# Optimization experiments

Hardware: AMD Instinct MI355X
Metric: run time of the kernel (lower is better)

The kernel has to match this reference:

```python
import jax, jax.numpy as jnp
import numpy as np
import math

ATTN_TEMP = 2.0


def _make_proj(p):
    # p: (B,2,4,4) -> combined (B,4,4): ext with top 3x4 replaced by K@ext[:3,:4]
    ext, intr = p[:, 0], p[:, 1]
    top = jnp.matmul(intr[:, :3, :3], ext[:, :3, :4])  # (B,3,4)
    return ext.at[:, :3, :4].set(top)


def _warp_grid(src_proj, ref_proj, depth):
    # returns pixel coords (ix, iy) each (B, D*H*W); matches torch homo_warping grid (no grad)
    B, D, H, W = depth.shape
    proj = jnp.matmul(src_proj, jnp.linalg.inv(ref_proj))  # (B,4,4)
    rot, trans = proj[:, :3, :3], proj[:, :3, 3:4]
    y, x = jnp.meshgrid(jnp.arange(H, dtype=jnp.float32), jnp.arange(W, dtype=jnp.float32), indexing='ij')
    xyz = jnp.stack([x.reshape(-1), y.reshape(-1), jnp.ones(H * W, jnp.float32)])  # (3,HW)
    rot_xyz = jnp.einsum('bij,jn->bin', rot, xyz)  # (B,3,HW)
    pxyz = rot_xyz[:, :, None, :] * depth.reshape(B, 1, D, H * W) + trans[:, :, :, None]  # (B,3,D,HW)
    z = pxyz[:, 2]
    z = jnp.where(z == 0, 1e-9, z)
    return jax.lax.stop_gradient((pxyz[:, 0] / z).reshape(B, -1)), jax.lax.stop_gradient((pxyz[:, 1] / z).reshape(B, -1))


def _bilinear_zeros(fea, ix_n, iy_n):
    # fea (B,C,Hs,Ws); ix_n,iy_n normalized [-1,1], align_corners=True, zero padding -> (B,C,N)
    B, C, Hs, Ws = fea.shape
    ix = (ix_n + 1.0) * ((Ws - 1) / 2.0)
    iy = (iy_n + 1.0) * ((Hs - 1) / 2.0)
    x0 = jnp.floor(ix); y0 = jnp.floor(iy)
    wx1 = ix - x0; wx0 = 1.0 - wx1
    wy1 = iy - y0; wy0 = 1.0 - wy1
    flat = fea.reshape(B, C, Hs * Ws)

    def tap(xi, yi, w):
        valid = (xi >= 0) & (xi < Ws) & (yi >= 0) & (yi < Hs)
        xc = jnp.clip(xi, 0, Ws - 1).astype(jnp.int32)
        yc = jnp.clip(yi, 0, Hs - 1).astype(jnp.int32)
        g = jnp.take_along_axis(flat, (yc * Ws + xc)[:, None, :], axis=2)  # (B,C,N)
        return g * (w * valid.astype(fea.dtype))[:, None, :]

    return (tap(x0, y0, wx0 * wy0) + tap(x0 + 1, y0, wx1 * wy0)
            + tap(x0, y0 + 1, wx0 * wy1) + tap(x0 + 1, y0 + 1, wx1 * wy1))


def _forward(ref_fea, src_feas, proj_matrices, depth_hypo, reg_w, G):
    B, C, H, W = ref_fea.shape
    D = depth_hypo.shape[1]
    Hs, Ws = src_feas.shape[-2:]
    ref_proj = _make_proj(proj_matrices[:, 0])
    ref_vol = ref_fea.reshape(B, G, C // G, 1, H, W)  # broadcast over depth
    cor_feats = jnp.zeros((B, G, D, H, W), ref_fea.dtype)
    cor_wsum = jnp.full((B, D, H, W), 1e-8, ref_fea.dtype)
    inv_sqrtC = 1.0 / math.sqrt(C)
    for v in range(src_feas.shape[0]):
        src_proj = _make_proj(proj_matrices[:, v + 1])
        ix, iy = _warp_grid(src_proj, ref_proj, depth_hypo)
        ixn = ix / ((Ws - 1) / 2.0) - 1.0
        iyn = iy / ((Hs - 1) / 2.0) - 1.0
        warped = _bilinear_zeros(src_feas[v], ixn, iyn).reshape(B, G, C // G, D, H, W)
        cor = (warped * ref_vol).mean(axis=2)  # (B,G,D,H,W) group correlation
        cw = jax.nn.softmax(cor.sum(axis=1) / ATTN_TEMP, axis=1) * inv_sqrtC  # (B,D,H,W)
        cor_wsum = cor_wsum + cw
        cor_feats = cor_feats + cw[:, None] * cor
    cor_feats = cor_feats / cor_wsum[:, None]
    logits = jnp.einsum('bgdhw,g->bdhw', cor_feats, reg_w)  # stand-in regnet
    attn = jax.nn.softmax(logits, axis=1)
    idx = jnp.argmax(attn, axis=1)  # (B,H,W)
    depth = jnp.take_along_axis(depth_hypo, idx[:, None], axis=1)[:, 0]
    return depth, attn


def setup_inputs() -> dict:
    key = jax.random.key(0)
    k1, k2, k3 = jax.random.split(key, 3)
    B, V, C, D, H, W = 2, 4, 32, 32, 128, 160
    ref_fea = jax.random.normal(k1, (B, C, H, W), jnp.float32)
    src_feas = jax.random.normal(k2, (V - 1, B, C, H, W), jnp.float32)
    # realistic camera matrices: shared intrinsics, src views offset by baselines
    K = np.eye(4, dtype=np.float32)
    K[0, 0] = K[1, 1] = 160.0; K[0, 2] = W / 2.0; K[1, 2] = H / 2.0
    proj = np.zeros((B, V, 2, 4, 4), np.float32)
    for b in range(B):
        for v in range(V):
            ext = np.eye(4, dtype=np.float32)
            if v > 0:
                ext[0, 3] = 15.0 * v * (1 if v % 2 else -1)
                ext[1, 3] = 5.0 * v
            proj[b, v, 0] = ext
            proj[b, v, 1] = K
    # depth planes 425..935 broadcast to (B,D,H,W)
    planes = np.linspace(425.0, 935.0, D, dtype=np.float32)
    depth_hypo = jnp.broadcast_to(jnp.asarray(planes)[None, :, None, None], (B, D, H, W)).copy()
    reg_w = jax.random.normal(k3, (8,), jnp.float32)
    return {"ref_fea": ref_fea, "src_feas": src_feas, "proj_matrices": jnp.asarray(proj),
            "depth_hypo": depth_hypo, "reg_w": reg_w, "group_cor_dim": 8}


def reference(ref_fea, src_feas, proj_matrices, depth_hypo, reg_w, group_cor_dim):
    return _forward(ref_fea, src_feas, proj_matrices, depth_hypo, reg_w, group_cor_dim)
```

## Files before the change

kernel.cpp:

```cpp
#include <hip/hip_runtime.h>

#define B_  2
#define V_  4
#define VS_ 3
#define C_  32
#define G_  8
#define D_  32
#define H_  128
#define W_  160
#define CELLS_MAX 128

__device__ void inv4x4(const float* m, float* out) {
    float a[4][8];
    for (int i = 0; i < 4; i++) {
        for (int j = 0; j < 4; j++) {
            a[i][j]     = m[i * 4 + j];
            a[i][j + 4] = (i == j) ? 1.f : 0.f;
        }
    }
    for (int c = 0; c < 4; c++) {
        int piv = c;
        float best = fabsf(a[c][c]);
        for (int r = c + 1; r < 4; r++) {
            float v = fabsf(a[r][c]);
            if (v > best) { best = v; piv = r; }
        }
        if (piv != c) {
            for (int j = 0; j < 8; j++) {
                float t = a[c][j]; a[c][j] = a[piv][j]; a[piv][j] = t;
            }
        }
        float pv = 1.f / a[c][c];
        for (int j = 0; j < 8; j++) a[c][j] *= pv;
        for (int r = 0; r < 4; r++) {
            if (r == c) continue;
            float f = a[r][c];
            for (int j = 0; j < 8; j++) a[r][j] -= f * a[c][j];
        }
    }
    for (int i = 0; i < 4; i++)
        for (int j = 0; j < 4; j++) out[i * 4 + j] = a[i][j + 4];
}

__device__ void make_proj(const float* p, float* o) {
    const float* ext = p;
    const float* K   = p + 16;
    for (int i = 0; i < 16; i++) o[i] = ext[i];
    for (int i = 0; i < 3; i++) {
        for (int j = 0; j < 4; j++) {
            float s = 0.f;
            for (int k = 0; k < 3; k++) s += K[i * 4 + k] * ext[k * 4 + j];
            o[i * 4 + j] = s;
        }
    }
}

__global__ void setup_proj_kernel(const float* __restrict__ proj,
                                  float* __restrict__ projp) {
    int t = threadIdx.x;
    if (t >= B_ * VS_) return;
    int b = t / VS_;
    int v = t % VS_ + 1;

    float refm[16], srcm[16], invr[16], P[16];
    make_proj(proj + ((size_t)(b * V_ + 0) * 2) * 16, refm);
    make_proj(proj + ((size_t)(b * V_ + v) * 2) * 16, srcm);
    inv4x4(refm, invr);
    for (int i = 0; i < 4; i++) {
        for (int j = 0; j < 4; j++) {
            float s = 0.f;
            for (int k = 0; k < 4; k++) s += srcm[i * 4 + k] * invr[k * 4 + j];
            P[i * 4 + j] = s;
        }
    }
    float* o = projp + t * 12;
    o[0] = P[0];  o[1] = P[1];  o[2]  = P[2];
    o[3] = P[4];  o[4] = P[5];  o[5]  = P[6];
    o[6] = P[8];  o[7] = P[9];  o[8]  = P[10];
    o[9] = P[3];  o[10] = P[7]; o[11] = P[11];
}

__global__ __launch_bounds__(256) void transpose_kernel(const float* __restrict__ in,
                                                        float* __restrict__ out) {
    __shared__ float tile[C_][W_ + 1];
    int n = blockIdx.x / H_;
    int y = blockIdx.x % H_;
    for (int idx = threadIdx.x; idx < C_ * W_; idx += 256) {
        int c = idx / W_;
        int x = idx - c * W_;
        tile[c][x] = in[(((size_t)n * C_ + c) * H_ + y) * W_ + x];
    }
    __syncthreads();
    float* op = out + ((size_t)n * H_ + y) * W_ * C_;
    for (int idx = threadIdx.x; idx < W_ * C_; idx += 256) {
        int c = idx & (C_ - 1);
        int x = idx >> 5;
        op[idx] = tile[c][x];
    }
}

__global__ __launch_bounds__(256, 8) void fused_kernel(const float* __restrict__ ref_fea,
                                                       const float* __restrict__ srcT,
                                                       const float* __restrict__ projp,
                                                       const float* __restrict__ depth_hypo,
                                                       const float* __restrict__ reg_w,
                                                       float* __restrict__ out) {
    const int WT = W_ / 8;
    int bid = blockIdx.x;
    int b   = bid / (H_ * WT);
    int rem = bid % (H_ * WT);
    int h   = rem / WT;
    int w0  = (rem % WT) * 8;

    int tid = threadIdx.x;
    int d   = tid & 31;
    int p   = tid >> 5;
    int w   = w0 + p;

    __shared__ float  s_ref[8][36];
    __shared__ float  s_depth[8][33];
    __shared__ float2 s_dot[2][8][CELLS_MAX];
    {
        int c  = tid >> 3;
        int px = tid & 7;
        s_ref[px][c]   = ref_fea[(((size_t)b * C_ + c) * H_ + h) * W_ + w0 + px];
        s_depth[px][c] = depth_hypo[(((size_t)b * D_ + c) * H_ + h) * W_ + w0 + px];
    }

    float rwv[G_];
#pragma unroll
    for (int g = 0; g < G_; ++g) rwv[g] = reg_w[g];

    __syncthreads();

    float depth = s_depth[p][d];
    float d_lo  = s_depth[p][0];
    float d_hi  = s_depth[p][31];
    float xf = (float)w, yf = (float)h;

    int xmn, ymn, nx, ny, nxp, shp;

    auto phase1 = [&](int v) {
        const float* M = projp + (b * VS_ + v) * 12;
        float rx = M[0] * xf + M[1] * yf + M[2];
        float ry = M[3] * xf + M[4] * yf + M[5];
        float rz = M[6] * xf + M[7] * yf + M[8];

        float Zl = rz * d_lo + M[11]; if (Zl == 0.f) Zl = 1e-9f;
        float Zh = rz * d_hi + M[11]; if (Zh == 0.f) Zh = 1e-9f;
        float il = 1.f / Zl, ih = 1.f / Zh;
        float xl = (rx * d_lo + M[9]) * il, yl = (ry * d_lo + M[10]) * il;
        float xh = (rx * d_hi + M[9]) * ih, yh = (ry * d_hi + M[10]) * ih;

        float xmnf = fminf(fmaxf(fminf(xl, xh), -2.f), (float)(W_ + 1));
        float xmxf = fminf(fmaxf(fmaxf(xl, xh), -2.f), (float)(W_ + 1));
        float ymnf = fminf(fmaxf(fminf(yl, yh), -2.f), (float)(H_ + 1));
        float ymxf = fminf(fmaxf(fmaxf(yl, yh), -2.f), (float)(H_ + 1));

        xmn = max((int)floorf(xmnf), -1);
        ymn = max((int)floorf(ymnf), -1);
        int xmx = min(max((int)floorf(xmxf), xmn), min(W_ - 1, xmn + 14));
        int ymx = min(max((int)floorf(ymxf), ymn), min(H_ - 1, ymn + 6));
        nx = xmx - xmn + 2;
        ny = ymx - ymn + 2;
        shp = (nx <= 4) ? 2 : ((nx <= 8) ? 3 : 4);
        nxp = 1 << shp;
        int ncp = nxp * ny;

        const float4* sp = (const float4*)(srcT + (size_t)(v * B_ + b) * H_ * W_ * C_);
        float2* dot = &s_dot[v & 1][p][0];
        for (int ci = d; ci < ncp; ci += 32) {
            int cx = ci & (nxp - 1);
            if (cx < nx) {
                int cy = ci >> shp;
                int sx = min(max(xmn + cx, 0), W_ - 1);
                int sy = min(max(ymn + cy, 0), H_ - 1);
                const float4* cp = sp + ((size_t)sy * W_ + sx) * (C_ / 4);
                float dS = 0.f, dR = 0.f;
#pragma unroll
                for (int q = 0; q < 8; ++q) {
                    float4 sv = cp[q];
                    float4 r  = *(const float4*)&s_ref[p][q * 4];
                    float gq = r.x * sv.x + r.y * sv.y + r.z * sv.z + r.w * sv.w;
                    dS += gq;
                    dR += rwv[q] * gq;
                }
                dot[ci] = make_float2(dS, dR);
            }
        }
    };

    float cwsum = 1e-8f;
    float acc   = 0.f;

    phase1(0);
    __syncthreads();

    for (int v = 0; v < VS_; ++v) {
        int cxmn = xmn, cymn = ymn, cnx = nx, cny = ny, cnxp = nxp;

        if (v + 1 < VS_) phase1(v + 1);

        const float* M = projp + (b * VS_ + v) * 12;
        float rx = M[0] * xf + M[1] * yf + M[2];
        float ry = M[3] * xf + M[4] * yf + M[5];
        float rz = M[6] * xf + M[7] * yf + M[8];
        float Z = rz * depth + M[11]; if (Z == 0.f) Z = 1e-9f;
        float iZ = 1.f / Z;
        float ix = (rx * depth + M[9]) * iZ;
        float iy = (ry * depth + M[10]) * iZ;
        float x0f = floorf(ix), y0f = floorf(iy);
        float wx1 = ix - x0f, wy1 = iy - y0f;
        float wx0 = 1.f - wx1, wy0 = 1.f - wy1;

        int x0 = (int)fminf(fmaxf(x0f, -2.f), (float)(W_ + 1));
        int y0 = (int)fminf(fmaxf(y0f, -2.f), (float)(H_ + 1));

        float vx0 = (x0f >= 0.f  && x0f <= (float)(W_ - 1)) ? 1.f : 0.f;
        float vx1 = (x0f >= -1.f && x0f <= (float)(W_ - 2)) ? 1.f : 0.f;
        float vy0 = (y0f >= 0.f  && y0f <= (float)(H_ - 1)) ? 1.f : 0.f;
        float vy1 = (y0f >= -1.f && y0f <= (float)(H_ - 2)) ? 1.f : 0.f;
        float ax0 = wx0 * vx0, ax1 = wx1 * vx1;
        float ay0 = wy0 * vy0, ay1 = wy1 * vy1;
        float w00 = ax0 * ay0, w10 = ax1 * ay0;
        float w01 = ax0 * ay1, w11 = ax1 * ay1;

        int cx0 = min(max(x0 - cxmn, 0), cnx - 2);
        int cy0 = min(max(y0 - cymn, 0), cny - 2);
        const float2* dot = &s_dot[v & 1][p][0];
        int cb = cy0 * cnxp + cx0;
        float2 d00 = dot[cb],        d10 = dot[cb + 1];
        float2 d01 = dot[cb + cnxp], d11 = dot[cb + cnxp + 1];
        float S = w00 * d00.x + w10 * d10.x + w01 * d01.x + w11 * d11.x;
        float R = w00 * d00.y + w10 * d10.y + w01 * d01.y + w11 * d11.y;

        float t = S * 0.125f;
        float m = t;
#pragma unroll
        for (int mask = 16; mask >= 1; mask >>= 1)
            m = fmaxf(m, __shfl_xor(m, mask));
        float e = __expf(t - m);
        float s = e;
#pragma unroll
        for (int mask = 16; mask >= 1; mask >>= 1)
            s += __shfl_xor(s, mask);
        float cw = e / s * 0.17677669529663689f;
        cwsum += cw;
        acc   += cw * (R * 0.25f);

        __syncthreads();
    }

    float logit = acc / cwsum;

    float m = logit;
#pragma unroll
    for (int mask = 16; mask >= 1; mask >>= 1)
        m = fmaxf(m, __shfl_xor(m, mask));
    float e = __expf(logit - m);
    float s = e;
#pragma unroll
    for (int mask = 16; mask >= 1; mask >>= 1)
        s += __shfl_xor(s, mask);
    float attn = e / s;

    float bv = logit;
    int   bi = d;
#pragma unroll
    for (int mask = 16; mask >= 1; mask >>= 1) {
        float ov = __shfl_xor(bv, mask);
        int   oi = __shfl_xor(bi, mask);
        if (ov > bv || (ov == bv && oi < bi)) { bv = ov; bi = oi; }
    }

    if (d == 0) {
        out[((size_t)b * H_ + h) * W_ + w] = s_depth[p][bi];
    }

    __shared__ float s_attn[8][33];
    s_attn[p][d] = attn;
    __syncthreads();
    int po = tid & 7;
    int d2 = tid >> 3;
    float* attn_out = out + (size_t)B_ * H_ * W_;
    attn_out[(((size_t)b * D_ + d2) * H_ + h) * W_ + w0 + po] = s_attn[po][d2];
}

extern "C" void kernel_launch(void* const* d_in, const int* in_sizes, int n_in,
                              void* d_out, int out_size, void* d_ws, size_t ws_size,
                              hipStream_t stream) {
    const float* ref_fea    = (const float*)d_in[0];
    const float* src_feas   = (const float*)d_in[1];
    const float* proj       = (const float*)d_in[2];
    const float* depth_hypo = (const float*)d_in[3];
    const float* reg_w      = (const float*)d_in[4];
    float* out = (float*)d_out;

    float* projp = (float*)d_ws;
    float* srcT  = projp + 256;

    setup_proj_kernel<<<1, 64, 0, stream>>>(proj, projp);
    transpose_kernel<<<VS_ * B_ * H_, 256, 0, stream>>>(src_feas, srcT);
    fused_kernel<<<B_ * H_ * (W_ / 8), 256, 0, stream>>>(ref_fea, srcT, projp,
                                                         depth_hypo, reg_w, out);
}
```

Before: 98.32 us.

## Stage block-wide source footprint in LDS and compute dots from shared memory

Each block now cooperatively loads the union footprint of source-view cells covering all 8 pixels (bounded by 24x8 cells) into shared memory, prefetching the next view into registers while the current one is processed. The per-pixel dot products then read source features from LDS instead of issuing redundant global float4 loads. This trades extra LDS (about 27KB), more syncs and register staging for less duplicated global traffic, and drops the occupancy hint from launch_bounds. Clamping the union box to 24x8 could truncate footprints if projections spread widely.

```diff
diff --git a/kernel.cpp b/kernel.cpp
--- a/kernel.cpp
+++ b/kernel.cpp
@@ -8,7 +8,10 @@
 #define D_  32
 #define H_  128
 #define W_  160
-#define CELLS_MAX 128
+#define UNX_ 24
+#define UNY_ 8
+#define CSTRIDE 9
+#define STAGE_IT 6
 
 __device__ void inv4x4(const float* m, float* out) {
     float a[4][8];
@@ -99,12 +102,12 @@
     }
 }
 
-__global__ __launch_bounds__(256, 8) void fused_kernel(const float* __restrict__ ref_fea,
-                                                       const float* __restrict__ srcT,
-                                                       const float* __restrict__ projp,
-                                                       const float* __restrict__ depth_hypo,
-                                                       const float* __restrict__ reg_w,
-                                                       float* __restrict__ out) {
+__global__ __launch_bounds__(256) void fused_kernel(const float* __restrict__ ref_fea,
+                                                    const float* __restrict__ srcT,
+                                                    const float* __restrict__ projp,
+                                                    const float* __restrict__ depth_hypo,
+                                                    const float* __restrict__ reg_w,
+                                                    float* __restrict__ out) {
     const int WT = W_ / 8;
     int bid = blockIdx.x;
     int b   = bid / (H_ * WT);
@@ -119,73 +122,138 @@
 
     __shared__ float  s_ref[8][36];
     __shared__ float  s_depth[8][33];
-    __shared__ float2 s_dot[2][8][CELLS_MAX];
+    __shared__ float2 s_dot[8][128];
+    __shared__ float4 s_U4[UNX_ * UNY_ * CSTRIDE];
+    __shared__ float  s_attn[8][33];
+
     {
         int c  = tid >> 3;
         int px = tid & 7;
         s_ref[px][c]   = ref_fea[(((size_t)b * C_ + c) * H_ + h) * W_ + w0 + px];
         s_depth[px][c] = depth_hypo[(((size_t)b * D_ + c) * H_ + h) * W_ + w0 + px];
     }
-
-    float rwv[G_];
-#pragma unroll
-    for (int g = 0; g < G_; ++g) rwv[g] = reg_w[g];
-
+    float rwq[G_];
+#pragma unroll
+    for (int g = 0; g < G_; ++g) rwq[g] = reg_w[g];
     __syncthreads();
 
     float depth = s_depth[p][d];
     float d_lo  = s_depth[p][0];
     float d_hi  = s_depth[p][31];
+    float dl0 = s_depth[0][0], dh0 = s_depth[0][31];
+    float dl7 = s_depth[7][0], dh7 = s_depth[7][31];
     float xf = (float)w, yf = (float)h;
 
-    int xmn, ymn, nx, ny, nxp, shp;
-
-    auto phase1 = [&](int v) {
+    int uxmn, uymn, unx, utot4;
+    float4 tmp[STAGE_IT];
+    int pxmn, pymn, pnx, pny, pnxp, pshp;
+
+    auto stage_load = [&](int v) {
         const float* M = projp + (b * VS_ + v) * 12;
-        float rx = M[0] * xf + M[1] * yf + M[2];
-        float ry = M[3] * xf + M[4] * yf + M[5];
-        float rz = M[6] * xf + M[7] * yf + M[8];
-
-        float Zl = rz * d_lo + M[11]; if (Zl == 0.f) Zl = 1e-9f;
-        float Zh = rz * d_hi + M[11]; if (Zh == 0.f) Zh = 1e-9f;
-        float il = 1.f / Zl, ih = 1.f / Zh;
-        float xl = (rx * d_lo + M[9]) * il, yl = (ry * d_lo + M[10]) * il;
-        float xh = (rx * d_hi + M[9]) * ih, yh = (ry * d_hi + M[10]) * ih;
-
+        float u0 = (float)w0, u1 = (float)(w0 + 7);
+        float rx0 = M[0]*u0 + M[1]*yf + M[2];
+        float ry0 = M[3]*u0 + M[4]*yf + M[5];
+        float rz0 = M[6]*u0 + M[7]*yf + M[8];
+        float rx1 = M[0]*u1 + M[1]*yf + M[2];
+        float ry1 = M[3]*u1 + M[4]*yf + M[5];
+        float rz1 = M[6]*u1 + M[7]*yf + M[8];
+
+        float cxs[4], cys[4];
+        {
+            float dd, Z, iZ;
+            dd = dl0; Z = rz0*dd + M[11]; if (Z == 0.f) Z = 1e-9f; iZ = 1.f/Z;
+            cxs[0] = (rx0*dd + M[9])*iZ; cys[0] = (ry0*dd + M[10])*iZ;
+            dd = dh0; Z = rz0*dd + M[11]; if (Z == 0.f) Z = 1e-9f; iZ = 1.f/Z;
+            cxs[1] = (rx0*dd + M[9])*iZ; cys[1] = (ry0*dd + M[10])*iZ;
+            dd = dl7; Z = rz1*dd + M[11]; if (Z == 0.f) Z = 1e-9f; iZ = 1.f/Z;
+            cxs[2] = (rx1*dd + M[9])*iZ; cys[2] = (ry1*dd + M[10])*iZ;
+            dd = dh7; Z = rz1*dd + M[11]; if (Z == 0.f) Z = 1e-9f; iZ = 1.f/Z;
+            cxs[3] = (rx1*dd + M[9])*iZ; cys[3] = (ry1*dd + M[10])*iZ;
+        }
+        float xmnf = fminf(fminf(cxs[0], cxs[1]), fminf(cxs[2], cxs[3]));
+        float xmxf = fmaxf(fmaxf(cxs[0], cxs[1]), fmaxf(cxs[2], cxs[3]));
+        float ymnf = fminf(fminf(cys[0], cys[1]), fminf(cys[2], cys[3]));
+        float ymxf = fmaxf(fmaxf(cys[0], cys[1]), fmaxf(cys[2], cys[3]));
+        xmnf = fminf(fmaxf(xmnf, -3.f), (float)(W_ + 2));
+        xmxf = fminf(fmaxf(xmxf, -3.f), (float)(W_ + 2));
+        ymnf = fminf(fmaxf(ymnf, -3.f), (float)(H_ + 2));
+        ymxf = fminf(fmaxf(ymxf, -3.f), (float)(H_ + 2));
+
+        uxmn = (int)floorf(xmnf) - 1;
+        int uxmx = (int)floorf(xmxf) + 2;
+        unx = min(uxmx - uxmn + 1, UNX_);
+        uymn = (int)floorf(ymnf) - 1;
+        int uymx = (int)floorf(ymxf) + 2;
+        int uny = min(uymx - uymn + 1, UNY_);
+        utot4 = unx * uny * 8;
+        float uinv = 1.f / (float)unx;
+
+        const float4* sp4 = (const float4*)(srcT + (size_t)(v * B_ + b) * H_ * W_ * C_);
+#pragma unroll
+        for (int k = 0; k < STAGE_IT; ++k) {
+            int idx = tid + k * 256;
+            if (idx < utot4) {
+                int cell = idx >> 3, q = idx & 7;
+                int cy = (int)(((float)cell + 0.5f) * uinv);
+                int cx = cell - cy * unx;
+                int sx = min(max(uxmn + cx, 0), W_ - 1);
+                int sy = min(max(uymn + cy, 0), H_ - 1);
+                tmp[k] = sp4[((size_t)sy * W_ + sx) * 8 + q];
+            }
+        }
+    };
+    auto stage_write = [&](int ) {
+#pragma unroll
+        for (int k = 0; k < STAGE_IT; ++k) {
+            int idx = tid + k * 256;
+            if (idx < utot4) {
+                int cell = idx >> 3, q = idx & 7;
+                s_U4[cell * CSTRIDE + q] = tmp[k];
+            }
+        }
+    };
+
+    auto dots = [&](int v) {
+        const float* M = projp + (b * VS_ + v) * 12;
+        float rx = M[0]*xf + M[1]*yf + M[2];
+        float ry = M[3]*xf + M[4]*yf + M[5];
+        float rz = M[6]*xf + M[7]*yf + M[8];
+        float Zl = rz*d_lo + M[11]; if (Zl == 0.f) Zl = 1e-9f;
+        float Zh = rz*d_hi + M[11]; if (Zh == 0.f) Zh = 1e-9f;
+        float il = 1.f/Zl, ih = 1.f/Zh;
+        float xl = (rx*d_lo + M[9])*il, yl = (ry*d_lo + M[10])*il;
+        float xh = (rx*d_hi + M[9])*ih, yh = (ry*d_hi + M[10])*ih;
         float xmnf = fminf(fmaxf(fminf(xl, xh), -2.f), (float)(W_ + 1));
         float xmxf = fminf(fmaxf(fmaxf(xl, xh), -2.f), (float)(W_ + 1));
         float ymnf = fminf(fmaxf(fminf(yl, yh), -2.f), (float)(H_ + 1));
         float ymxf = fminf(fmaxf(fmaxf(yl, yh), -2.f), (float)(H_ + 1));
-
-        xmn = max((int)floorf(xmnf), -1);
-        ymn = max((int)floorf(ymnf), -1);
-        int xmx = min(max((int)floorf(xmxf), xmn), min(W_ - 1, xmn + 14));
-        int ymx = min(max((int)floorf(ymxf), ymn), min(H_ - 1, ymn + 6));
-        nx = xmx - xmn + 2;
-        ny = ymx - ymn + 2;
-        shp = (nx <= 4) ? 2 : ((nx <= 8) ? 3 : 4);
-        nxp = 1 << shp;
-        int ncp = nxp * ny;
-
-        const float4* sp = (const float4*)(srcT + (size_t)(v * B_ + b) * H_ * W_ * C_);
-        float2* dot = &s_dot[v & 1][p][0];
+        pxmn = max((int)floorf(xmnf), -1);
+        pymn = max((int)floorf(ymnf), -1);
+        int xmx = min(max((int)floorf(xmxf), pxmn), min(W_ - 1, pxmn + 14));
+        int ymx = min(max((int)floorf(ymxf), pymn), min(H_ - 1, pymn + 6));
+        pnx = xmx - pxmn + 2;
+        pny = ymx - pymn + 2;
+        pshp = (pnx <= 4) ? 2 : ((pnx <= 8) ? 3 : 4);
+        pnxp = 1 << pshp;
+        int ncp = pnxp * pny;
+        int ox = pxmn - uxmn;
+        int oy = pymn - uymn;
+
         for (int ci = d; ci < ncp; ci += 32) {
-            int cx = ci & (nxp - 1);
-            if (cx < nx) {
-                int cy = ci >> shp;
-                int sx = min(max(xmn + cx, 0), W_ - 1);
-                int sy = min(max(ymn + cy, 0), H_ - 1);
-                const float4* cp = sp + ((size_t)sy * W_ + sx) * (C_ / 4);
+            int cx = ci & (pnxp - 1);
+            if (cx < pnx) {
+                int cy = ci >> pshp;
+                int b4 = ((oy + cy) * unx + (ox + cx)) * CSTRIDE;
                 float dS = 0.f, dR = 0.f;
 #pragma unroll
                 for (int q = 0; q < 8; ++q) {
-                    float4 sv = cp[q];
+                    float4 sv = s_U4[b4 + q];
                     float4 r  = *(const float4*)&s_ref[p][q * 4];
-                    float gq = r.x * sv.x + r.y * sv.y + r.z * sv.z + r.w * sv.w;
+                    float gq = r.x*sv.x + r.y*sv.y + r.z*sv.z + r.w*sv.w;
                     dS += gq;
-                    dR += rwv[q] * gq;
+                    dR += rwq[q] * gq;
                 }
-                dot[ci] = make_float2(dS, dR);
+                s_dot[p][ci] = make_float2(dS, dR);
             }
         }
     };
@@ -193,22 +261,15 @@
     float cwsum = 1e-8f;
     float acc   = 0.f;
 
-    phase1(0);
-    __syncthreads();
-
-    for (int v = 0; v < VS_; ++v) {
-        int cxmn = xmn, cymn = ymn, cnx = nx, cny = ny, cnxp = nxp;
-
-        if (v + 1 < VS_) phase1(v + 1);
-
+    auto phase2 = [&](int v) {
         const float* M = projp + (b * VS_ + v) * 12;
-        float rx = M[0] * xf + M[1] * yf + M[2];
-        float ry = M[3] * xf + M[4] * yf + M[5];
-        float rz = M[6] * xf + M[7] * yf + M[8];
-        float Z = rz * depth + M[11]; if (Z == 0.f) Z = 1e-9f;
+        float rx = M[0]*xf + M[1]*yf + M[2];
+        float ry = M[3]*xf + M[4]*yf + M[5];
+        float rz = M[6]*xf + M[7]*yf + M[8];
+        float Z = rz*depth + M[11]; if (Z == 0.f) Z = 1e-9f;
         float iZ = 1.f / Z;
-        float ix = (rx * depth + M[9]) * iZ;
-        float iy = (ry * depth + M[10]) * iZ;
+        float ix = (rx*depth + M[9]) * iZ;
+        float iy = (ry*depth + M[10]) * iZ;
         float x0f = floorf(ix), y0f = floorf(iy);
         float wx1 = ix - x0f, wy1 = iy - y0f;
         float wx0 = 1.f - wx1, wy0 = 1.f - wy1;
@@ -225,14 +286,13 @@
         float w00 = ax0 * ay0, w10 = ax1 * ay0;
         float w01 = ax0 * ay1, w11 = ax1 * ay1;
 
-        int cx0 = min(max(x0 - cxmn, 0), cnx - 2);
-        int cy0 = min(max(y0 - cymn, 0), cny - 2);
-        const float2* dot = &s_dot[v & 1][p][0];
-        int cb = cy0 * cnxp + cx0;
-        float2 d00 = dot[cb],        d10 = dot[cb + 1];
-        float2 d01 = dot[cb + cnxp], d11 = dot[cb + cnxp + 1];
-        float S = w00 * d00.x + w10 * d10.x + w01 * d01.x + w11 * d11.x;
-        float R = w00 * d00.y + w10 * d10.y + w01 * d01.y + w11 * d11.y;
+        int cx0 = min(max(x0 - pxmn, 0), pnx - 2);
+        int cy0 = min(max(y0 - pymn, 0), pny - 2);
+        int cb  = cy0 * pnxp + cx0;
+        float2 d00 = s_dot[p][cb],        d10 = s_dot[p][cb + 1];
+        float2 d01 = s_dot[p][cb + pnxp], d11 = s_dot[p][cb + pnxp + 1];
+        float S = w00*d00.x + w10*d10.x + w01*d01.x + w11*d11.x;
+        float R = w00*d00.y + w10*d10.y + w01*d01.y + w11*d11.y;
 
         float t = S * 0.125f;
         float m = t;
@@ -247,9 +307,24 @@
         float cw = e / s * 0.17677669529663689f;
         cwsum += cw;
         acc   += cw * (R * 0.25f);
-
-        __syncthreads();
-    }
+    };
+
+    stage_load(0); stage_write(0);
+    __syncthreads();
+    dots(0);
+    stage_load(1);
+    phase2(0);
+    __syncthreads();
+    stage_write(1);
+    __syncthreads();
+    dots(1);
+    stage_load(2);
+    phase2(1);
+    __syncthreads();
+    stage_write(2);
+    __syncthreads();
+    dots(2);
+    phase2(2);
 
     float logit = acc / cwsum;
 
@@ -277,7 +352,6 @@
         out[((size_t)b * H_ + h) * W_ + w] = s_depth[p][bi];
     }
 
-    __shared__ float s_attn[8][33];
     s_attn[p][d] = attn;
     __syncthreads();
     int po = tid & 7;
```

After: 106.2 us. +8.0%, slower.
